# Optimization experiments

Measured on AMD Instinct MI355X. Metric: run time of the kernel, lower is better.

The kernel has to match this reference:

```python
import jax, jax.numpy as jnp
import numpy as np

B, D, DEPTH, C = 8192, 2048, 10, 1000
NUM_INNER = 2 ** DEPTH - 1   # 1023
NUM_LEAVES = 2 ** DEPTH      # 1024


def setup_inputs() -> dict:
    key = jax.random.key(0)
    k1, k2, k3, k4 = jax.random.split(key, 4)
    x = jax.random.normal(k1, (B, D), dtype=jnp.float32)
    # scale weights like a typical init so sigmoid isn't fully saturated
    W = jax.random.normal(k2, (D, NUM_INNER), dtype=jnp.float32) * 0.02
    b = jax.random.normal(k3, (NUM_INNER,), dtype=jnp.float32) * 0.02
    leaf_dist = jax.random.normal(k4, (NUM_LEAVES, C), dtype=jnp.float32)
    return {"x": x, "W": W, "b": b, "leaf_dist": leaf_dist}


def reference(x, W, b, leaf_dist):
    # inner node routing probabilities: [B, num_inner]
    decisions = jax.nn.sigmoid(x @ W + b)
    depth = int(np.log2(decisions.shape[1] + 1))
    pp = jnp.ones((x.shape[0], 1), dtype=x.dtype)  # path probs, starts at root
    for d in range(depth):  # small fixed loop over tree depth
        s, e = 2 ** d - 1, 2 ** (d + 1) - 1
        ld = decisions[:, s:e]                      # [B, 2^d]
        pp = jnp.concatenate([pp * ld, pp * (1.0 - ld)], axis=1)  # [B, 2^(d+1)]
        # faithful reproduction of the original's even/odd reordering
        pp = jnp.concatenate([pp[:, ::2], pp[:, 1::2]], axis=1)
    leaf_probs = jax.nn.softmax(leaf_dist, axis=1)  # [num_leaves, C]
    return pp @ leaf_probs                          # [B, C]
```

## Files before the change

### kernel.cpp

```cpp
#include <hip/hip_runtime.h>

typedef __attribute__((ext_vector_type(8))) unsigned short ushort8v;
typedef __attribute__((ext_vector_type(8))) __bf16 bf16x8;
typedef __attribute__((ext_vector_type(4))) float floatx4;

__device__ __forceinline__ unsigned short f2b(float f) {
    unsigned u = __float_as_uint(f);
    unsigned r = u + 0x7fffu + ((u >> 16) & 1u);
    return (unsigned short)(r >> 16);
}
__device__ __forceinline__ float b2f(unsigned short h) {
    return __uint_as_float(((unsigned)h) << 16);
}


__global__ __launch_bounds__(256) void prep_kernel(const float* __restrict__ x,
                                                   unsigned short* __restrict__ A2x,
                                                   const float* __restrict__ W,
                                                   unsigned short* __restrict__ B2w,
                                                   const float* __restrict__ ld_,
                                                   unsigned short* __restrict__ B2p) {
    __shared__ float tile[32 * 33];
    __shared__ float buf[1000];
    __shared__ float red[8];
    const int b = blockIdx.x, t = threadIdx.x;
    if (b < 2048) {
        const int mt = b >> 2, kq = (b & 3) * 64;
        const int kco = t >> 4, l16 = t & 15;
        const float* xr0 = x + (size_t)(mt * 16 + l16) * 2048;
#pragma unroll
        for (int i = 0; i < 4; i++) {
            const int kc = kq + i * 16 + kco;
            const float* xr = xr0 + kc * 8;
            float4 v0 = *(const float4*)xr;
            float4 v1 = *(const float4*)(xr + 4);
            ushort8v o;
            o[0] = f2b(v0.x); o[1] = f2b(v0.y); o[2] = f2b(v0.z); o[3] = f2b(v0.w);
            o[4] = f2b(v1.x); o[5] = f2b(v1.y); o[6] = f2b(v1.z); o[7] = f2b(v1.w);
            *(ushort8v*)(A2x + ((size_t)(mt * 256 + kc) * 16 + l16) * 8) = o;
        }
    } else if (b < 4096) {
        const int idx = b - 2048;
        const int n0 = (idx & 31) * 32, k0 = (idx >> 5) * 32;
        const int tx = t & 31, ty = t >> 5;
#pragma unroll
        for (int i = 0; i < 4; i++) {
            int k = k0 + ty + i * 8, n = n0 + tx;
            tile[(ty + i * 8) * 33 + tx] = (n < 1023) ? W[(size_t)k * 1023 + n] : 0.f;
        }
        __syncthreads();
#pragma unroll
        for (int i = 0; i < 4; i++) {
            int n = n0 + ty + i * 8, k = k0 + tx;
            size_t off = ((size_t)((n >> 4) * 256 + (k >> 3)) * 16 + (n & 15)) * 8 + (k & 7);
            B2w[off] = f2b(tile[tx * 33 + ty + i * 8]);
        }
    } else {
        const int l0 = b - 4096;
        const float* r = ld_ + (size_t)l0 * 1000;
        float mx = -3.4e38f;
        for (int i = t; i < 1000; i += 256) { float v = r[i]; buf[i] = v; mx = fmaxf(mx, v); }
#pragma unroll
        for (int o = 32; o > 0; o >>= 1) mx = fmaxf(mx, __shfl_down(mx, o));
        if ((t & 63) == 0) red[t >> 6] = mx;
        __syncthreads();
        mx = fmaxf(fmaxf(red[0], red[1]), fmaxf(red[2], red[3]));
        float s = 0.f;
        for (int i = t; i < 1000; i += 256) { float e = __expf(buf[i] - mx); buf[i] = e; s += e; }
#pragma unroll
        for (int o = 32; o > 0; o >>= 1) s += __shfl_down(s, o);
        if ((t & 63) == 0) red[4 + (t >> 6)] = s;
        __syncthreads();
        float inv = 1.f / (red[4] + red[5] + red[6] + red[7]);
        for (int i = t; i < 1024; i += 256) {
            float pv = (i < 1000) ? buf[i] * inv : 0.f;
            size_t off = ((size_t)((i >> 4) * 128 + (l0 >> 3)) * 16 + (i & 15)) * 8 + (l0 & 7);
            B2p[off] = f2b(pv);
        }
    }
}

__global__ __launch_bounds__(256) void pp_kernel(const unsigned short* __restrict__ dec,
                                                 unsigned short* __restrict__ A2p) {
    __shared__ unsigned short dsh[8 * 1024];
    __shared__ float pa[8 * 1024];
    __shared__ float pb[8 * 1024];
    const int t = threadIdx.x;
    const int r0 = blockIdx.x * 8;
    {
        const ushort8v* src = (const ushort8v*)(dec + (size_t)r0 * 1024);
        ushort8v* dst = (ushort8v*)dsh;
        for (int g = t; g < 1024; g += 256) dst[g] = src[g];
    }
    if (t < 8) pa[t * 1024] = 1.f;
    __syncthreads();
    float* cur = pa; float* nxt = pb;
    for (int dep = 0; dep < 10; dep++) {
        const int half = 1 << dep;
        const int len  = half << 1;
        const int total = len << 3;
        for (int idx = t; idx < total; idx += 256) {
            const int r = idx >> (dep + 1);
            const int j = idx & (len - 1);
            int tt = j >> dep;
            int s  = j & (half - 1);
            int i2 = 2 * s + tt;
            int u  = i2 >> dep;
            int rr = i2 & (half - 1);
            float dv = b2f(dsh[r * 1024 + half - 1 + rr]);
            nxt[r * 1024 + j] = cur[r * 1024 + rr] * (u ? (1.f - dv) : dv);
        }
        __syncthreads();
        float* tmp = cur; cur = nxt; nxt = tmp;
    }
    for (int i = t; i < 8192; i += 256) {
        const int r = i >> 10, j = i & 1023;
        const int rrow = r0 + r;
        size_t off = ((size_t)((rrow >> 4) * 128 + (j >> 3)) * 16 + (rrow & 15)) * 8 + (j & 7);
        A2p[off] = f2b(cur[r * 1024 + j]);
    }
}

template <int EPI>
__global__ __launch_bounds__(128, 2) void gemm_frag(const unsigned short* __restrict__ A2,
                                                    const unsigned short* __restrict__ B2,
                                                    const float* __restrict__ bias,
                                                    unsigned short* __restrict__ obf,
                                                    float* __restrict__ of32,
                                                    int KC, int ldo) {
    const int tid  = threadIdx.x;
    const int lane = tid & 63;
    const int wave = tid >> 6;
    const int quad = lane >> 4, l16 = lane & 15;

    const int l   = blockIdx.x;
    const int xcd = l & 7;
    const int j   = l >> 3;
    const int bm  = xcd * 8 + (j & 7);
    const int bn  = j >> 3;

    const int mt0 = bm * 8 + wave * 4;
    const int nt0 = bn * 8;

    const int lofs = (quad * 16 + l16) * 8;
    const unsigned short* ap[4];
    const unsigned short* bp[8];
#pragma unroll
    for (int mi = 0; mi < 4; mi++) ap[mi] = A2 + (size_t)(mt0 + mi) * KC * 128 + lofs;
#pragma unroll
    for (int ni = 0; ni < 8; ni++) bp[ni] = B2 + (size_t)(nt0 + ni) * KC * 128 + lofs;

    floatx4 acc[4][8] = {};
    const int NIT = KC >> 2;

    bf16x8 a0[4], b0[8], a1[4], b1[8];
#pragma unroll
    for (int mi = 0; mi < 4; mi++)
        a0[mi] = __builtin_bit_cast(bf16x8, *(const ushort8v*)(ap[mi]));
#pragma unroll
    for (int ni = 0; ni < 8; ni++)
        b0[ni] = __builtin_bit_cast(bf16x8, *(const ushort8v*)(bp[ni]));

    for (int it = 0; it < NIT; it += 2) {
        {
            const size_t ko = (size_t)(it + 1) * 512;
#pragma unroll
            for (int mi = 0; mi < 4; mi++)
                a1[mi] = __builtin_bit_cast(bf16x8, *(const ushort8v*)(ap[mi] + ko));
#pragma unroll
            for (int ni = 0; ni < 8; ni++)
                b1[ni] = __builtin_bit_cast(bf16x8, *(const ushort8v*)(bp[ni] + ko));
        }
#pragma unroll
        for (int mi = 0; mi < 4; mi++)
#pragma unroll
            for (int ni = 0; ni < 8; ni++)
                acc[mi][ni] = __builtin_amdgcn_mfma_f32_16x16x32_bf16(
                    a0[mi], b0[ni], acc[mi][ni], 0, 0, 0);
        if (it + 2 < NIT) {
            const size_t ko = (size_t)(it + 2) * 512;
#pragma unroll
            for (int mi = 0; mi < 4; mi++)
                a0[mi] = __builtin_bit_cast(bf16x8, *(const ushort8v*)(ap[mi] + ko));
#pragma unroll
            for (int ni = 0; ni < 8; ni++)
                b0[ni] = __builtin_bit_cast(bf16x8, *(const ushort8v*)(bp[ni] + ko));
        }
#pragma unroll
        for (int mi = 0; mi < 4; mi++)
#pragma unroll
            for (int ni = 0; ni < 8; ni++)
                acc[mi][ni] = __builtin_amdgcn_mfma_f32_16x16x32_bf16(
                    a1[mi], b1[ni], acc[mi][ni], 0, 0, 0);
    }

#pragma unroll
    for (int ni = 0; ni < 8; ni++) {
        const int col = (nt0 + ni) * 16 + l16;
        float bb = 0.f;
        if constexpr (EPI == 0) bb = (col < 1023) ? bias[col] : 0.f;
#pragma unroll
        for (int mi = 0; mi < 4; mi++) {
            const int row0 = (mt0 + mi) * 16 + quad * 4;
#pragma unroll
            for (int r = 0; r < 4; r++) {
                float v = acc[mi][ni][r];
                if constexpr (EPI == 0) {
                    float sgm = 1.f / (1.f + __expf(-(v + bb)));
                    obf[(size_t)(row0 + r) * ldo + col] = f2b(sgm);
                } else {
                    if (col < 1000) of32[(size_t)(row0 + r) * ldo + col] = v;
                }
            }
        }
    }
}

extern "C" void kernel_launch(void* const* d_in, const int* in_sizes, int n_in,
                              void* d_out, int out_size, void* d_ws, size_t ws_size,
                              hipStream_t stream) {
    const float* x   = (const float*)d_in[0];
    const float* W   = (const float*)d_in[1];
    const float* b   = (const float*)d_in[2];
    const float* ldd = (const float*)d_in[3];
    float* out = (float*)d_out;

    char* ws = (char*)d_ws;
    unsigned short* A2x = (unsigned short*)(ws);
    unsigned short* A2p = (unsigned short*)(ws);
    unsigned short* B2w = (unsigned short*)(ws + 33554432);
    unsigned short* dec = (unsigned short*)(ws + 37748736);
    unsigned short* B2p = (unsigned short*)(ws + 54525952);

    prep_kernel<<<5120, 256, 0, stream>>>(x, A2x, W, B2w, ldd, B2p);
    gemm_frag<0><<<512, 128, 0, stream>>>(A2x, B2w, b, dec, nullptr, 256, 1024);
    pp_kernel<<<1024, 256, 0, stream>>>(dec, A2p);
    gemm_frag<1><<<512, 128, 0, stream>>>(A2p, B2p, nullptr, nullptr, out, 128, 1000);
}
```

Before: 214.7 us.

## Stage GEMM tiles in LDS via direct global-to-LDS loads with double buffering

Replaces the register-direct GEMM, where each wave loaded its own A and B fragments from global memory, with a 256-thread block that cooperatively copies 128x128 A/B tiles into double-buffered LDS using global_load_lds. Each of the four waves then computes a 64x64 sub-tile from the LDS fragments. This shares tile loads across waves and cuts redundant global traffic. In exchange it adds a block-wide barrier per K step, uses 64KB of LDS per block (which may limit occupancy), and shrinks the per-wave accumulator tile.

```diff
diff --git a/kernel.cpp b/kernel.cpp
--- a/kernel.cpp
+++ b/kernel.cpp
@@ -11,6 +11,13 @@
 }
 __device__ __forceinline__ float b2f(unsigned short h) {
     return __uint_as_float(((unsigned)h) << 16);
+}
+
+__device__ __forceinline__ void gload16(const unsigned short* g, unsigned short* l) {
+    __builtin_amdgcn_global_load_lds(
+        (const __attribute__((address_space(1))) unsigned int*)g,
+        (__attribute__((address_space(3))) unsigned int*)l,
+        16, 0, 0);
 }
 
 
@@ -122,16 +129,20 @@
 }
 
 template <int EPI>
-__global__ __launch_bounds__(128, 2) void gemm_frag(const unsigned short* __restrict__ A2,
-                                                    const unsigned short* __restrict__ B2,
-                                                    const float* __restrict__ bias,
-                                                    unsigned short* __restrict__ obf,
-                                                    float* __restrict__ of32,
-                                                    int KC, int ldo) {
+__global__ __launch_bounds__(256, 2) void gemm_lds(const unsigned short* __restrict__ A2,
+                                                   const unsigned short* __restrict__ B2,
+                                                   const float* __restrict__ bias,
+                                                   unsigned short* __restrict__ obf,
+                                                   float* __restrict__ of32,
+                                                   int KC, int ldo) {
+    __shared__ unsigned short ldsA[2][8192];
+    __shared__ unsigned short ldsB[2][8192];
+
     const int tid  = threadIdx.x;
     const int lane = tid & 63;
     const int wave = tid >> 6;
     const int quad = lane >> 4, l16 = lane & 15;
+    const int wr = wave >> 1, wc = wave & 1;
 
     const int l   = blockIdx.x;
     const int xcd = l & 7;
@@ -139,72 +150,75 @@
     const int bm  = xcd * 8 + (j & 7);
     const int bn  = j >> 3;
 
-    const int mt0 = bm * 8 + wave * 4;
-    const int nt0 = bn * 8;
-
-    const int lofs = (quad * 16 + l16) * 8;
-    const unsigned short* ap[4];
-    const unsigned short* bp[8];
-#pragma unroll
-    for (int mi = 0; mi < 4; mi++) ap[mi] = A2 + (size_t)(mt0 + mi) * KC * 128 + lofs;
-#pragma unroll
-    for (int ni = 0; ni < 8; ni++) bp[ni] = B2 + (size_t)(nt0 + ni) * KC * 128 + lofs;
-
-    floatx4 acc[4][8] = {};
-    const int NIT = KC >> 2;
-
-    bf16x8 a0[4], b0[8], a1[4], b1[8];
-#pragma unroll
-    for (int mi = 0; mi < 4; mi++)
-        a0[mi] = __builtin_bit_cast(bf16x8, *(const ushort8v*)(ap[mi]));
-#pragma unroll
-    for (int ni = 0; ni < 8; ni++)
-        b0[ni] = __builtin_bit_cast(bf16x8, *(const ushort8v*)(bp[ni]));
-
-    for (int it = 0; it < NIT; it += 2) {
-        {
-            const size_t ko = (size_t)(it + 1) * 512;
-#pragma unroll
-            for (int mi = 0; mi < 4; mi++)
-                a1[mi] = __builtin_bit_cast(bf16x8, *(const ushort8v*)(ap[mi] + ko));
-#pragma unroll
-            for (int ni = 0; ni < 8; ni++)
-                b1[ni] = __builtin_bit_cast(bf16x8, *(const ushort8v*)(bp[ni] + ko));
-        }
-#pragma unroll
-        for (int mi = 0; mi < 4; mi++)
-#pragma unroll
-            for (int ni = 0; ni < 8; ni++)
-                acc[mi][ni] = __builtin_amdgcn_mfma_f32_16x16x32_bf16(
-                    a0[mi], b0[ni], acc[mi][ni], 0, 0, 0);
-        if (it + 2 < NIT) {
-            const size_t ko = (size_t)(it + 2) * 512;
-#pragma unroll
-            for (int mi = 0; mi < 4; mi++)
-                a0[mi] = __builtin_bit_cast(bf16x8, *(const ushort8v*)(ap[mi] + ko));
-#pragma unroll
-            for (int ni = 0; ni < 8; ni++)
-                b0[ni] = __builtin_bit_cast(bf16x8, *(const ushort8v*)(bp[ni] + ko));
-        }
-#pragma unroll
-        for (int mi = 0; mi < 4; mi++)
-#pragma unroll
-            for (int ni = 0; ni < 8; ni++)
-                acc[mi][ni] = __builtin_amdgcn_mfma_f32_16x16x32_bf16(
-                    a1[mi], b1[ni], acc[mi][ni], 0, 0, 0);
-    }
-
-#pragma unroll
-    for (int ni = 0; ni < 8; ni++) {
-        const int col = (nt0 + ni) * 16 + l16;
+    const int cBase = tid >> 4;
+    const int sub   = (tid & 15) * 8;
+    const unsigned short* srcA[4];
+    const unsigned short* srcB[4];
+#pragma unroll
+    for (int i = 0; i < 4; i++) {
+        const int c  = i * 16 + cBase;
+        const int mi = c >> 3, kcq = c & 7;
+        srcA[i] = A2 + ((size_t)(bm * 8 + mi) * KC + kcq) * 128 + sub;
+        srcB[i] = B2 + ((size_t)(bn * 8 + mi) * KC + kcq) * 128 + sub;
+    }
+
+    floatx4 acc[4][4] = {};
+    const int nks = KC >> 3;
+
+#pragma unroll
+    for (int i = 0; i < 4; i++) {
+        const int c = i * 16 + cBase;
+        gload16(srcA[i], &ldsA[0][c * 128 + sub]);
+        gload16(srcB[i], &ldsB[0][c * 128 + sub]);
+    }
+    __syncthreads();
+
+    int buf = 0;
+    for (int ks = 0; ks < nks; ks++) {
+        if (ks + 1 < nks) {
+            const size_t ko = (size_t)(ks + 1) * 1024;
+#pragma unroll
+            for (int i = 0; i < 4; i++) {
+                const int c = i * 16 + cBase;
+                gload16(srcA[i] + ko, &ldsA[buf ^ 1][c * 128 + sub]);
+                gload16(srcB[i] + ko, &ldsB[buf ^ 1][c * 128 + sub]);
+            }
+        }
+#pragma unroll
+        for (int kk = 0; kk < 2; kk++) {
+            bf16x8 af[4], bfv[4];
+#pragma unroll
+            for (int m2 = 0; m2 < 4; m2++)
+                af[m2] = __builtin_bit_cast(bf16x8,
+                    *(const ushort8v*)&ldsA[buf][((wr * 4 + m2) * 8 + kk * 4 + quad) * 128 + l16 * 8]);
+#pragma unroll
+            for (int n2 = 0; n2 < 4; n2++)
+                bfv[n2] = __builtin_bit_cast(bf16x8,
+                    *(const ushort8v*)&ldsB[buf][((wc * 4 + n2) * 8 + kk * 4 + quad) * 128 + l16 * 8]);
+#pragma unroll
+            for (int m2 = 0; m2 < 4; m2++)
+#pragma unroll
+                for (int n2 = 0; n2 < 4; n2++)
+                    acc[m2][n2] = __builtin_amdgcn_mfma_f32_16x16x32_bf16(
+                        af[m2], bfv[n2], acc[m2][n2], 0, 0, 0);
+        }
+        __syncthreads();
+        buf ^= 1;
+    }
+
+    const int mt0 = bm * 8 + wr * 4;
+    const int nt0 = bn * 8 + wc * 4;
+#pragma unroll
+    for (int n2 = 0; n2 < 4; n2++) {
+        const int col = (nt0 + n2) * 16 + l16;
         float bb = 0.f;
         if constexpr (EPI == 0) bb = (col < 1023) ? bias[col] : 0.f;
 #pragma unroll
-        for (int mi = 0; mi < 4; mi++) {
-            const int row0 = (mt0 + mi) * 16 + quad * 4;
+        for (int m2 = 0; m2 < 4; m2++) {
+            const int row0 = (mt0 + m2) * 16 + quad * 4;
 #pragma unroll
             for (int r = 0; r < 4; r++) {
-                float v = acc[mi][ni][r];
+                float v = acc[m2][n2][r];
                 if constexpr (EPI == 0) {
                     float sgm = 1.f / (1.f + __expf(-(v + bb)));
                     obf[(size_t)(row0 + r) * ldo + col] = f2b(sgm);
@@ -233,7 +247,7 @@
     unsigned short* B2p = (unsigned short*)(ws + 54525952);
 
     prep_kernel<<<5120, 256, 0, stream>>>(x, A2x, W, B2w, ldd, B2p);
-    gemm_frag<0><<<512, 128, 0, stream>>>(A2x, B2w, b, dec, nullptr, 256, 1024);
+    gemm_lds<0><<<512, 256, 0, stream>>>(A2x, B2w, b, dec, nullptr, 256, 1024);
     pp_kernel<<<1024, 256, 0, stream>>>(dec, A2p);
-    gemm_frag<1><<<512, 128, 0, stream>>>(A2p, B2p, nullptr, nullptr, out, 128, 1000);
-}
+    gemm_lds<1><<<512, 256, 0, stream>>>(A2p, B2p, nullptr, nullptr, out, 128, 1000);
+}
```

After: 202.6 us. 5.7% less time.
